# Performance work log

Hardware: AMD Instinct MI355X
Metric: run time of the kernel (lower is better)

## Reference

```python
import jax, jax.numpy as jnp
import numpy as np

B, T, C, H = 8, 2048, 1024, 1024
SCALE = 1.0 / np.sqrt(H).astype(np.float32)


def setup_inputs() -> dict:
    key = jax.random.key(0)
    kx, kq, kk, kv = jax.random.split(key, 4)
    x = jax.random.normal(kx, (B, T, C), dtype=jnp.float32)
    # Linear(C -> H, bias=False): store weights as [C, H] so y = x @ W
    Wq = jax.random.normal(kq, (C, H), dtype=jnp.float32) * (1.0 / np.sqrt(C))
    Wk = jax.random.normal(kk, (C, H), dtype=jnp.float32) * (1.0 / np.sqrt(C))
    Wv = jax.random.normal(kv, (C, H), dtype=jnp.float32) * (1.0 / np.sqrt(C))
    return {"x": x, "Wq": Wq, "Wk": Wk, "Wv": Wv}


def reference(x, Wq, Wk, Wv):
    # Projections
    Q = jnp.einsum('btc,ch->bth', x, Wq)
    K = jnp.einsum('btc,ch->bth', x, Wk)
    V = jnp.einsum('btc,ch->bth', x, Wv)
    t = x.shape[1]
    # Scaled dot-product scores with causal mask
    attn = jnp.einsum('bqh,bkh->bqk', Q, K) * SCALE  # [B,T,T]
    causal = jnp.tril(jnp.ones((t, t), dtype=bool))
    attn = jnp.where(causal, attn, -jnp.inf)
    scores = jax.nn.softmax(attn, axis=-1)
    # dropout p=0.0 (eval/deterministic) -> identity
    out = jnp.einsum('bqk,bkh->bqh', scores, V)
    return out
```

## Files before the change

kernel.cpp:

```cpp
#include <hip/hip_runtime.h>


typedef __attribute__((ext_vector_type(8))) __bf16 bf16x8;
typedef __attribute__((ext_vector_type(4))) float floatx4;

__device__ __forceinline__ unsigned short f2bf(float f) {
  unsigned int u = __float_as_uint(f);
  u += 0x7fffu + ((u >> 16) & 1u);
  return (unsigned short)(u >> 16);
}
__device__ __forceinline__ float bf2f(unsigned short s) {
  return __uint_as_float(((unsigned int)s) << 16);
}

__device__ __forceinline__ void gload_lds16(const unsigned short* g, unsigned short* l) {
  __builtin_amdgcn_global_load_lds(
      (const __attribute__((address_space(1))) void*)g,
      (__attribute__((address_space(3))) void*)l,
      16, 0, 0);
}

__device__ __forceinline__ void gemm_mainloop64(
    const unsigned short* __restrict__ A, int lda,
    const unsigned short* __restrict__ Bt, int ldb,
    int m0, int n0, int kSteps,
    unsigned short* As, unsigned short* Bs,
    floatx4 (&acc)[4][4])
{
  const int tid  = threadIdx.x;
  const int wave = tid >> 6;
  const int lane = tid & 63;
  const int wr = wave >> 1;
  const int wc = wave & 1;

  const int rowIn = lane >> 3;
  const int srcChunk = (((lane & 7) ^ rowIn) << 3);

  const unsigned short* gA = A  + (size_t)(m0 + wave * 32 + rowIn) * lda + srcChunk;
  const unsigned short* gB = Bt + (size_t)(n0 + wave * 32 + rowIn) * ldb + srcChunk;
  const int lda8 = lda << 3;
  const int ldb8 = ldb << 3;

  const int fr = lane & 15;
  const int kq = lane >> 4;
  const int ac0 = ((kq ^ (fr & 7)) << 3);
  const int ac1 = (((4 + kq) ^ (fr & 7)) << 3);

  for (int kt = 0; kt < kSteps; ++kt) {
    __syncthreads();
#pragma unroll
    for (int i = 0; i < 4; ++i)
      gload_lds16(gA + i * lda8, As + (wave * 32 + i * 8) * 64);
#pragma unroll
    for (int i = 0; i < 4; ++i)
      gload_lds16(gB + i * ldb8, Bs + (wave * 32 + i * 8) * 64);
    gA += 64; gB += 64;
    __syncthreads();

    bf16x8 af[4], bg[4];
#pragma unroll
    for (int i = 0; i < 4; ++i)
      af[i] = *(const bf16x8*)(As + (wr * 64 + i * 16 + fr) * 64 + ac0);
#pragma unroll
    for (int j = 0; j < 4; ++j)
      bg[j] = *(const bf16x8*)(Bs + (wc * 64 + j * 16 + fr) * 64 + ac0);
#pragma unroll
    for (int i = 0; i < 4; ++i)
#pragma unroll
      for (int j = 0; j < 4; ++j)
        acc[i][j] = __builtin_amdgcn_mfma_f32_16x16x32_bf16(af[i], bg[j], acc[i][j], 0, 0, 0);
#pragma unroll
    for (int i = 0; i < 4; ++i)
      af[i] = *(const bf16x8*)(As + (wr * 64 + i * 16 + fr) * 64 + ac1);
#pragma unroll
    for (int j = 0; j < 4; ++j)
      bg[j] = *(const bf16x8*)(Bs + (wc * 64 + j * 16 + fr) * 64 + ac1);
#pragma unroll
    for (int i = 0; i < 4; ++i)
#pragma unroll
      for (int j = 0; j < 4; ++j)
        acc[i][j] = __builtin_amdgcn_mfma_f32_16x16x32_bf16(af[i], bg[j], acc[i][j], 0, 0, 0);
  }
}

#define ACC_INIT(acc)                         \
  do {                                        \
    floatx4 z_ = {0.f, 0.f, 0.f, 0.f};        \
    _Pragma("unroll")                         \
    for (int i_ = 0; i_ < 4; ++i_)            \
      _Pragma("unroll")                       \
      for (int j_ = 0; j_ < 4; ++j_)          \
        acc[i_][j_] = z_;                     \
  } while (0)


__global__ __launch_bounds__(256) void prep_kernel(
    const float* __restrict__ x,
    const float* __restrict__ Wq,
    const float* __restrict__ Wk,
    const float* __restrict__ Wv,
    unsigned short* __restrict__ xb,
    unsigned short* __restrict__ Wt,
    float* __restrict__ l)
{
  const int bid = blockIdx.x;
  const int tid = threadIdx.x;
  if (bid < 16384) {
    int idx = (bid * 256 + tid) * 4;
    float4 v = *(const float4*)(x + idx);
    ushort4 o;
    o.x = f2bf(v.x); o.y = f2bf(v.y); o.z = f2bf(v.z); o.w = f2bf(v.w);
    *(ushort4*)(xb + idx) = o;
  } else if (bid < 17152) {
    __shared__ unsigned short tile[64][65];
    const int wb = bid - 16384;
    const float* W = (wb < 256) ? Wq : (wb < 512) ? Wk : Wv;
    unsigned short* Wtp = Wt + (size_t)(wb >> 8) * 1048576;
    const int rem = wb & 255;
    const int k0 = (rem & 15) * 64, n0 = (rem >> 4) * 64;
    const int tx = tid & 63, ty = tid >> 6;
#pragma unroll
    for (int r = 0; r < 64; r += 4)
      tile[r + ty][tx] = f2bf(W[(size_t)(k0 + r + ty) * 1024 + (n0 + tx)]);
    __syncthreads();
#pragma unroll
    for (int r = 0; r < 64; r += 4)
      Wtp[(size_t)(n0 + r + ty) * 1024 + (k0 + tx)] = tile[tx][r + ty];
  } else {
    l[(bid - 17152) * 256 + tid] = 0.f;
  }
}

__global__ __launch_bounds__(512, 2) void gemm_qkv_kernel(
    const unsigned short* __restrict__ xb,
    const unsigned short* __restrict__ Wt,
    unsigned short* __restrict__ Q,
    unsigned short* __restrict__ K,
    unsigned short* __restrict__ V)
{
  __shared__ __align__(16) unsigned short lds[49152];

  const int bid = blockIdx.x;
  const int xcd = bid & 7;
  const int local = bid >> 3;
  const int mi = xcd * 8 + (local & 7);
  const int ni = local >> 3;
  const int m0 = mi * 256;
  const int n0 = ni * 256;

  const int tid = threadIdx.x;
  const int w = tid >> 6;
  const int l = tid & 63;
  const int wr = w >> 2;
  const int wc = w & 3;

  const int sr0 = w * 16 + (l >> 2);
  const int scs = (((l & 3) ^ ((l >> 3) & 3)) << 3);

  const unsigned short* pA0 = xb + (size_t)(m0 + sr0) * 1024 + scs;
  const unsigned short* pA1 = xb + (size_t)(m0 + 128 + sr0) * 1024 + scs;
  const unsigned short* pB0 = Wt + (size_t)(n0 + sr0) * 1024 + scs;
  const unsigned short* pB1 = Wt + (size_t)(n0 + 128 + sr0) * 1024 + scs;

  const int stgW = w * 512;

#define STAGE4(slot)                                             \
  do {                                                           \
    unsigned short* _sA = &lds[(slot) * 8192 + stgW];            \
    unsigned short* _sB = &lds[24576 + (slot) * 8192 + stgW];    \
    gload_lds16(pA0, _sA);                                       \
    gload_lds16(pA1, _sA + 4096);                                \
    gload_lds16(pB0, _sB);                                       \
    gload_lds16(pB1, _sB + 4096);                                \
    pA0 += 32; pA1 += 32; pB0 += 32; pB1 += 32;                  \
  } while (0)

  const int fr = l & 15;
  const int q  = l >> 4;
  const int cks = ((q ^ ((fr >> 1) & 3)) << 3);
  const int aOff = (wr * 128 + fr) * 32 + cks;
  const int bOff = (wc * 64 + fr) * 32 + cks;

  floatx4 acc[8][4];
  {
    floatx4 z = {0.f, 0.f, 0.f, 0.f};
#pragma unroll
    for (int i = 0; i < 8; ++i)
#pragma unroll
      for (int j = 0; j < 4; ++j)
        acc[i][j] = z;
  }

  STAGE4(0);
  STAGE4(1);
  asm volatile("s_waitcnt vmcnt(4)" ::: "memory");
  __builtin_amdgcn_s_barrier();

  bf16x8 a[8], b0[4], b1[4];
  {
    const unsigned short* sA = &lds[0];
    const unsigned short* sB = &lds[24576];
#pragma unroll
    for (int j = 0; j < 4; ++j) b0[j] = *(const bf16x8*)(sB + bOff + j * 512);
    a[0] = *(const bf16x8*)(sA + aOff);
    a[1] = *(const bf16x8*)(sA + aOff + 512);
  }

#define MFMA_PAIR(I0, BU)                                                           \
  do {                                                                              \
    __builtin_amdgcn_s_setprio(1);                                                  \
    _Pragma("unroll")                                                               \
    for (int j = 0; j < 4; ++j) {                                                   \
      acc[(I0)][j] =                                                                \
          __builtin_amdgcn_mfma_f32_16x16x32_bf16(a[(I0)], BU[j], acc[(I0)][j], 0, 0, 0); \
      acc[(I0) + 1][j] =                                                            \
          __builtin_amdgcn_mfma_f32_16x16x32_bf16(a[(I0) + 1], BU[j], acc[(I0) + 1][j], 0, 0, 0); \
    }                                                                               \
    __builtin_amdgcn_s_setprio(0);                                                  \
  } while (0)

#define ITER(KT, BU, BP)                                                  \
  do {                                                                    \
    const int nslot = (slot == 2) ? 0 : slot + 1;                         \
    const int sslot = (nslot == 2) ? 0 : nslot + 1;                       \
    const unsigned short* sA  = &lds[slot * 8192];                        \
    const unsigned short* sAn = &lds[nslot * 8192];                       \
    const unsigned short* sBn = &lds[24576 + nslot * 8192];               \
    unsigned short* dA = &lds[sslot * 8192 + stgW];                       \
    unsigned short* dB = &lds[24576 + sslot * 8192 + stgW];               \
    const bool doStage = ((KT) < 30);                                     \
    const bool doNext  = ((KT) < 31);                                     \
    a[2] = *(const bf16x8*)(sA + aOff + 2 * 512);                         \
    a[3] = *(const bf16x8*)(sA + aOff + 3 * 512);                         \
    if (doStage) gload_lds16(pA0, dA);                                    \
    __builtin_amdgcn_s_barrier();                                         \
    MFMA_PAIR(0, BU);                                                     \
    __builtin_amdgcn_s_barrier();                                         \
    a[4] = *(const bf16x8*)(sA + aOff + 4 * 512);                         \
    a[5] = *(const bf16x8*)(sA + aOff + 5 * 512);                         \
    if (doStage) gload_lds16(pA1, dA + 4096);                             \
    __builtin_amdgcn_s_barrier();                                         \
    MFMA_PAIR(2, BU);                                                     \
    __builtin_amdgcn_s_barrier();                                         \
    a[6] = *(const bf16x8*)(sA + aOff + 6 * 512);                         \
    a[7] = *(const bf16x8*)(sA + aOff + 7 * 512);                         \
    if (doStage) gload_lds16(pB0, dB);                                    \
    __builtin_amdgcn_s_barrier();                                         \
    MFMA_PAIR(4, BU);                                                     \
    __builtin_amdgcn_s_barrier();                                         \
    if (doStage) STAGE_LAST(dB);                                          \
    if (doNext) {                                                         \
      if (doStage) asm volatile("s_waitcnt vmcnt(3)" ::: "memory");       \
      else         asm volatile("s_waitcnt vmcnt(0)" ::: "memory");       \
      __builtin_amdgcn_s_barrier();                                       \
      _Pragma("unroll")                                                   \
      for (int j = 0; j < 4; ++j)                                         \
        BP[j] = *(const bf16x8*)(sBn + bOff + j * 512);                   \
      a[0] = *(const bf16x8*)(sAn + aOff);                                \
      a[1] = *(const bf16x8*)(sAn + aOff + 512);                          \
    }                                                                     \
    MFMA_PAIR(6, BU);                                                     \
    __builtin_amdgcn_s_barrier();                                         \
    slot = nslot;                                                         \
  } while (0)

#define STAGE_LAST(dB)                                                    \
  do {                                                                    \
    gload_lds16(pB1, (dB) + 4096);                                        \
    pA0 += 32; pA1 += 32; pB0 += 32; pB1 += 32;                           \
  } while (0)

  int slot = 0;
#pragma unroll 1
  for (int kt2 = 0; kt2 < 16; ++kt2) {
    const int kt = kt2 * 2;
    ITER(kt, b0, b1);
    ITER(kt + 1, b1, b0);
  }
#undef ITER
#undef STAGE_LAST
#undef MFMA_PAIR
#undef STAGE4

  unsigned short* const dsts[3] = {Q, K, V};
  unsigned short* D = dsts[n0 >> 10];
  const int ncol0 = n0 & 1023;

  const int rb = m0 + wr * 128 + (q << 2);
  const int cb = ncol0 + wc * 64 + fr;
#pragma unroll
  for (int i = 0; i < 8; ++i)
#pragma unroll
    for (int j = 0; j < 4; ++j)
#pragma unroll
      for (int r = 0; r < 4; ++r)
        D[(size_t)(rb + i * 16 + r) * 1024 + (cb + j * 16)] = f2bf(acc[i][j][r]);
}

__global__ void transpose_v_kernel(const unsigned short* __restrict__ V,
                                   unsigned short* __restrict__ Vt) {
  __shared__ unsigned short tile[64][68];
  const int b = blockIdx.z;
  const int t0 = blockIdx.x * 64, h0 = blockIdx.y * 64;
  const int tid = threadIdx.x;
  const int cx = (tid & 15) * 4;
  const int ry = tid >> 4;
  const unsigned short* Vb = V + (size_t)b * 2048 * 1024;
#pragma unroll
  for (int r = 0; r < 64; r += 16) {
    ushort4 v = *(const ushort4*)(Vb + (size_t)(t0 + r + ry) * 1024 + (h0 + cx));
    *(ushort4*)&tile[r + ry][cx] = v;
  }
  __syncthreads();
  unsigned short* Vtb = Vt + (size_t)b * 1024 * 2048;
#pragma unroll
  for (int r = 0; r < 64; r += 16) {
    const int h = r + ry;
    ushort4 o;
    o.x = tile[cx][h]; o.y = tile[cx + 1][h]; o.z = tile[cx + 2][h]; o.w = tile[cx + 3][h];
    *(ushort4*)(Vtb + (size_t)(h0 + h) * 2048 + (t0 + cx)) = o;
  }
}

__global__ __launch_bounds__(256) void gemm_scores_kernel(
    const unsigned short* __restrict__ Q,
    const unsigned short* __restrict__ K,
    unsigned short* __restrict__ S,
    float* __restrict__ lsum)
{
  const int b = blockIdx.x & 7;
  const int t = blockIdx.x >> 3;
  int mi = (int)((sqrtf(8.f * (float)t + 1.f) - 1.f) * 0.5f);
  while ((mi + 1) * (mi + 2) / 2 <= t) ++mi;
  while (mi * (mi + 1) / 2 > t) --mi;
  const int ni = t - mi * (mi + 1) / 2;
  const int m0 = mi * 128;
  const int n0 = ni * 128;

  __shared__ __align__(16) unsigned short As[128 * 64];
  __shared__ __align__(16) unsigned short Bs[128 * 64];
  floatx4 acc[4][4];
  ACC_INIT(acc);
  const unsigned short* Qb = Q + (size_t)b * 2048 * 1024;
  const unsigned short* Kb = K + (size_t)b * 2048 * 1024;
  gemm_mainloop64(Qb, 1024, Kb, 1024, m0, n0, 16, As, Bs, acc);

  unsigned short* Sb = S + (size_t)b * 2048 * 2048;
  float* lb = lsum + b * 2048;
  const int tid = threadIdx.x, wave = tid >> 6, lane = tid & 63;
  const int wr = wave >> 1, wc = wave & 1;
  const int rb = m0 + wr * 64 + ((lane >> 4) << 2);
  const int cb = n0 + wc * 64 + (lane & 15);

  float rsum[4][4];
#pragma unroll
  for (int i = 0; i < 4; ++i)
#pragma unroll
    for (int r = 0; r < 4; ++r)
      rsum[i][r] = 0.f;

#pragma unroll
  for (int i = 0; i < 4; ++i)
#pragma unroll
    for (int j = 0; j < 4; ++j)
#pragma unroll
      for (int r = 0; r < 4; ++r) {
        const int tq = rb + i * 16 + r;
        const int tk = cb + j * 16;
        float e = 0.f;
        if (tk <= tq) e = __expf(acc[i][j][r] * 0.03125f);
        const unsigned short h = f2bf(e);
        Sb[(size_t)tq * 2048 + tk] = h;
        rsum[i][r] += bf2f(h);
      }

#pragma unroll
  for (int off = 1; off < 16; off <<= 1)
#pragma unroll
    for (int i = 0; i < 4; ++i)
#pragma unroll
      for (int r = 0; r < 4; ++r)
        rsum[i][r] += __shfl_xor(rsum[i][r], off, 64);

  if ((lane & 15) == 0) {
#pragma unroll
    for (int i = 0; i < 4; ++i)
#pragma unroll
      for (int r = 0; r < 4; ++r)
        atomicAdd(&lb[rb + i * 16 + r], rsum[i][r]);
  }
}

__global__ __launch_bounds__(256) void gemm_pv_kernel(
    const unsigned short* __restrict__ S,
    const unsigned short* __restrict__ Vt,
    const float* __restrict__ lsum,
    float* __restrict__ out)
{
  const int b = blockIdx.x & 7;
  const int r2 = blockIdx.x >> 3;
  const int mi = 15 - (r2 >> 3);
  const int ni = r2 & 7;
  const int m0 = mi * 128;
  const int n0 = ni * 128;

  __shared__ __align__(16) unsigned short As[128 * 64];
  __shared__ __align__(16) unsigned short Bs[128 * 64];
  floatx4 acc[4][4];
  ACC_INIT(acc);
  const unsigned short* Pb = S  + (size_t)b * 2048 * 2048;
  const unsigned short* Vb = Vt + (size_t)b * 1024 * 2048;
  const int kSteps = m0 / 64 + 2;
  gemm_mainloop64(Pb, 2048, Vb, 2048, m0, n0, kSteps, As, Bs, acc);

  float* Ob = out + (size_t)b * 2048 * 1024;
  const float* lb = lsum + b * 2048;
  const int tid = threadIdx.x, wave = tid >> 6, lane = tid & 63;
  const int wr = wave >> 1, wc = wave & 1;
  const int rb = m0 + wr * 64 + ((lane >> 4) << 2);
  const int cb = n0 + wc * 64 + (lane & 15);

  float inv[4][4];
#pragma unroll
  for (int i = 0; i < 4; ++i)
#pragma unroll
    for (int r = 0; r < 4; ++r)
      inv[i][r] = 1.0f / lb[rb + i * 16 + r];

#pragma unroll
  for (int i = 0; i < 4; ++i)
#pragma unroll
    for (int j = 0; j < 4; ++j)
#pragma unroll
      for (int r = 0; r < 4; ++r)
        Ob[(size_t)(rb + i * 16 + r) * 1024 + (cb + j * 16)] = acc[i][j][r] * inv[i][r];
}


extern "C" void kernel_launch(void* const* d_in, const int* in_sizes, int n_in,
                              void* d_out, int out_size, void* d_ws, size_t ws_size,
                              hipStream_t stream) {
  const float* x  = (const float*)d_in[0];
  const float* Wq = (const float*)d_in[1];
  const float* Wk = (const float*)d_in[2];
  const float* Wv = (const float*)d_in[3];
  float* out = (float*)d_out;

  char* ws = (char*)d_ws;
  unsigned short* xb  = (unsigned short*)(ws);
  unsigned short* Wt  = (unsigned short*)(ws + 33554432ull);
  unsigned short* Q   = (unsigned short*)(ws + 39845888ull);
  unsigned short* K   = (unsigned short*)(ws + 73400320ull);
  unsigned short* V   = (unsigned short*)(ws + 106954752ull);
  unsigned short* Vt  = (unsigned short*)(ws + 140509184ull);
  unsigned short* S   = (unsigned short*)(ws + 174063616ull);
  float*          l   = (float*)(ws + 241172480ull);

  prep_kernel<<<17216, 256, 0, stream>>>(x, Wq, Wk, Wv, xb, Wt, l);

  gemm_qkv_kernel<<<768, 512, 0, stream>>>(xb, Wt, Q, K, V);

  transpose_v_kernel<<<dim3(32, 16, 8), 256, 0, stream>>>(V, Vt);
  gemm_scores_kernel<<<8 * 136, 256, 0, stream>>>(Q, K, S, l);
  gemm_pv_kernel<<<1024, 256, 0, stream>>>(S, Vt, l, out);
}
```

Baseline: 350.7 us.

## Fuse V transpose into QKV epilogue and widen PV tiles to 128x256

The QKV GEMM epilogue now writes V directly in transposed layout (Vt), so the separate transpose kernel and its extra read and write of V are gone. The PV GEMM switches to 512-thread blocks with 128x256 output tiles through a new mainloop variant, which halves the block count and reuses each loaded P tile across twice as many columns. The transposed stores are 8-byte ushort4 writes strided by 2048 elements, so they coalesce worse than the old row-major stores. The larger PV tiles also reduce parallelism for the causal workload.

```diff
diff --git a/kernel.cpp b/kernel.cpp
--- a/kernel.cpp
+++ b/kernel.cpp
@@ -54,6 +54,69 @@
 #pragma unroll
     for (int i = 0; i < 4; ++i)
       gload_lds16(gB + i * ldb8, Bs + (wave * 32 + i * 8) * 64);
+    gA += 64; gB += 64;
+    __syncthreads();
+
+    bf16x8 af[4], bg[4];
+#pragma unroll
+    for (int i = 0; i < 4; ++i)
+      af[i] = *(const bf16x8*)(As + (wr * 64 + i * 16 + fr) * 64 + ac0);
+#pragma unroll
+    for (int j = 0; j < 4; ++j)
+      bg[j] = *(const bf16x8*)(Bs + (wc * 64 + j * 16 + fr) * 64 + ac0);
+#pragma unroll
+    for (int i = 0; i < 4; ++i)
+#pragma unroll
+      for (int j = 0; j < 4; ++j)
+        acc[i][j] = __builtin_amdgcn_mfma_f32_16x16x32_bf16(af[i], bg[j], acc[i][j], 0, 0, 0);
+#pragma unroll
+    for (int i = 0; i < 4; ++i)
+      af[i] = *(const bf16x8*)(As + (wr * 64 + i * 16 + fr) * 64 + ac1);
+#pragma unroll
+    for (int j = 0; j < 4; ++j)
+      bg[j] = *(const bf16x8*)(Bs + (wc * 64 + j * 16 + fr) * 64 + ac1);
+#pragma unroll
+    for (int i = 0; i < 4; ++i)
+#pragma unroll
+      for (int j = 0; j < 4; ++j)
+        acc[i][j] = __builtin_amdgcn_mfma_f32_16x16x32_bf16(af[i], bg[j], acc[i][j], 0, 0, 0);
+  }
+}
+
+__device__ __forceinline__ void gemm_mainloop64w(
+    const unsigned short* __restrict__ A, int lda,
+    const unsigned short* __restrict__ Bt, int ldb,
+    int m0, int n0, int kSteps,
+    unsigned short* As, unsigned short* Bs,
+    floatx4 (&acc)[4][4])
+{
+  const int tid  = threadIdx.x;
+  const int w    = tid >> 6;
+  const int lane = tid & 63;
+  const int wr = w >> 2;
+  const int wc = w & 3;
+
+  const int rowIn = lane >> 3;
+  const int srcChunk = (((lane & 7) ^ rowIn) << 3);
+
+  const unsigned short* gA = A  + (size_t)(m0 + w * 16 + rowIn) * lda + srcChunk;
+  const unsigned short* gB = Bt + (size_t)(n0 + w * 32 + rowIn) * ldb + srcChunk;
+  const int lda8 = lda << 3;
+  const int ldb8 = ldb << 3;
+
+  const int fr = lane & 15;
+  const int kq = lane >> 4;
+  const int ac0 = ((kq ^ (fr & 7)) << 3);
+  const int ac1 = (((4 + kq) ^ (fr & 7)) << 3);
+
+  for (int kt = 0; kt < kSteps; ++kt) {
+    __syncthreads();
+#pragma unroll
+    for (int i = 0; i < 2; ++i)
+      gload_lds16(gA + i * lda8, As + (w * 16 + i * 8) * 64);
+#pragma unroll
+    for (int i = 0; i < 4; ++i)
+      gload_lds16(gB + i * ldb8, Bs + (w * 32 + i * 8) * 64);
     gA += 64; gB += 64;
     __syncthreads();
 
@@ -136,7 +199,7 @@
     const unsigned short* __restrict__ Wt,
     unsigned short* __restrict__ Q,
     unsigned short* __restrict__ K,
-    unsigned short* __restrict__ V)
+    unsigned short* __restrict__ Vt)
 {
   __shared__ __align__(16) unsigned short lds[49152];
 
@@ -248,7 +311,10 @@
     __builtin_amdgcn_s_barrier();                                         \
     MFMA_PAIR(4, BU);                                                     \
     __builtin_amdgcn_s_barrier();                                         \
-    if (doStage) STAGE_LAST(dB);                                          \
+    if (doStage) {                                                        \
+      gload_lds16(pB1, dB + 4096);                                        \
+      pA0 += 32; pA1 += 32; pB0 += 32; pB1 += 32;                         \
+    }                                                                     \
     if (doNext) {                                                         \
       if (doStage) asm volatile("s_waitcnt vmcnt(3)" ::: "memory");       \
       else         asm volatile("s_waitcnt vmcnt(0)" ::: "memory");       \
@@ -264,12 +330,6 @@
     slot = nslot;                                                         \
   } while (0)
 
-#define STAGE_LAST(dB)                                                    \
-  do {                                                                    \
-    gload_lds16(pB1, (dB) + 4096);                                        \
-    pA0 += 32; pA1 += 32; pB0 += 32; pB1 += 32;                           \
-  } while (0)
-
   int slot = 0;
 #pragma unroll 1
   for (int kt2 = 0; kt2 < 16; ++kt2) {
@@ -278,47 +338,34 @@
     ITER(kt + 1, b1, b0);
   }
 #undef ITER
-#undef STAGE_LAST
 #undef MFMA_PAIR
 #undef STAGE4
 
-  unsigned short* const dsts[3] = {Q, K, V};
-  unsigned short* D = dsts[n0 >> 10];
-  const int ncol0 = n0 & 1023;
-
   const int rb = m0 + wr * 128 + (q << 2);
-  const int cb = ncol0 + wc * 64 + fr;
-#pragma unroll
-  for (int i = 0; i < 8; ++i)
-#pragma unroll
-    for (int j = 0; j < 4; ++j)
-#pragma unroll
-      for (int r = 0; r < 4; ++r)
-        D[(size_t)(rb + i * 16 + r) * 1024 + (cb + j * 16)] = f2bf(acc[i][j][r]);
-}
-
-__global__ void transpose_v_kernel(const unsigned short* __restrict__ V,
-                                   unsigned short* __restrict__ Vt) {
-  __shared__ unsigned short tile[64][68];
-  const int b = blockIdx.z;
-  const int t0 = blockIdx.x * 64, h0 = blockIdx.y * 64;
-  const int tid = threadIdx.x;
-  const int cx = (tid & 15) * 4;
-  const int ry = tid >> 4;
-  const unsigned short* Vb = V + (size_t)b * 2048 * 1024;
-#pragma unroll
-  for (int r = 0; r < 64; r += 16) {
-    ushort4 v = *(const ushort4*)(Vb + (size_t)(t0 + r + ry) * 1024 + (h0 + cx));
-    *(ushort4*)&tile[r + ry][cx] = v;
-  }
-  __syncthreads();
-  unsigned short* Vtb = Vt + (size_t)b * 1024 * 2048;
-#pragma unroll
-  for (int r = 0; r < 64; r += 16) {
-    const int h = r + ry;
-    ushort4 o;
-    o.x = tile[cx][h]; o.y = tile[cx + 1][h]; o.z = tile[cx + 2][h]; o.w = tile[cx + 3][h];
-    *(ushort4*)(Vtb + (size_t)(h0 + h) * 2048 + (t0 + cx)) = o;
+  const int cbl = wc * 64 + fr;
+  if (n0 < 2048) {
+    unsigned short* D = (n0 < 1024) ? Q : K;
+    const int cb = (n0 & 1023) + cbl;
+#pragma unroll
+    for (int i = 0; i < 8; ++i)
+#pragma unroll
+      for (int j = 0; j < 4; ++j)
+#pragma unroll
+        for (int r = 0; r < 4; ++r)
+          D[(size_t)(rb + i * 16 + r) * 1024 + (cb + j * 16)] = f2bf(acc[i][j][r]);
+  } else {
+    const size_t bb = (size_t)(rb >> 11) * (1024ull * 2048ull);
+    const int t0 = rb & 2047;
+    const int h0 = (n0 - 2048) + cbl;
+#pragma unroll
+    for (int i = 0; i < 8; ++i)
+#pragma unroll
+      for (int j = 0; j < 4; ++j) {
+        ushort4 o;
+        o.x = f2bf(acc[i][j][0]); o.y = f2bf(acc[i][j][1]);
+        o.z = f2bf(acc[i][j][2]); o.w = f2bf(acc[i][j][3]);
+        *(ushort4*)(Vt + bb + (size_t)(h0 + j * 16) * 2048 + (t0 + i * 16)) = o;
+      }
   }
 }
 
@@ -391,7 +438,7 @@
   }
 }
 
-__global__ __launch_bounds__(256) void gemm_pv_kernel(
+__global__ __launch_bounds__(512) void gemm_pv_kernel(
     const unsigned short* __restrict__ S,
     const unsigned short* __restrict__ Vt,
     const float* __restrict__ lsum,
@@ -399,24 +446,24 @@
 {
   const int b = blockIdx.x & 7;
   const int r2 = blockIdx.x >> 3;
-  const int mi = 15 - (r2 >> 3);
-  const int ni = r2 & 7;
+  const int mi = 15 - (r2 >> 2);
+  const int ni = r2 & 3;
   const int m0 = mi * 128;
-  const int n0 = ni * 128;
+  const int n0 = ni * 256;
 
   __shared__ __align__(16) unsigned short As[128 * 64];
-  __shared__ __align__(16) unsigned short Bs[128 * 64];
+  __shared__ __align__(16) unsigned short Bs[256 * 64];
   floatx4 acc[4][4];
   ACC_INIT(acc);
   const unsigned short* Pb = S  + (size_t)b * 2048 * 2048;
   const unsigned short* Vb = Vt + (size_t)b * 1024 * 2048;
   const int kSteps = m0 / 64 + 2;
-  gemm_mainloop64(Pb, 2048, Vb, 2048, m0, n0, kSteps, As, Bs, acc);
+  gemm_mainloop64w(Pb, 2048, Vb, 2048, m0, n0, kSteps, As, Bs, acc);
 
   float* Ob = out + (size_t)b * 2048 * 1024;
   const float* lb = lsum + b * 2048;
-  const int tid = threadIdx.x, wave = tid >> 6, lane = tid & 63;
-  const int wr = wave >> 1, wc = wave & 1;
+  const int tid = threadIdx.x, w = tid >> 6, lane = tid & 63;
+  const int wr = w >> 2, wc = w & 3;
   const int rb = m0 + wr * 64 + ((lane >> 4) << 2);
   const int cb = n0 + wc * 64 + (lane & 15);
 
@@ -451,16 +498,14 @@
   unsigned short* Wt  = (unsigned short*)(ws + 33554432ull);
   unsigned short* Q   = (unsigned short*)(ws + 39845888ull);
   unsigned short* K   = (unsigned short*)(ws + 73400320ull);
-  unsigned short* V   = (unsigned short*)(ws + 106954752ull);
-  unsigned short* Vt  = (unsigned short*)(ws + 140509184ull);
-  unsigned short* S   = (unsigned short*)(ws + 174063616ull);
-  float*          l   = (float*)(ws + 241172480ull);
+  unsigned short* Vt  = (unsigned short*)(ws + 106954752ull);
+  unsigned short* S   = (unsigned short*)(ws + 140509184ull);
+  float*          l   = (float*)(ws + 207618048ull);
 
   prep_kernel<<<17216, 256, 0, stream>>>(x, Wq, Wk, Wv, xb, Wt, l);
 
-  gemm_qkv_kernel<<<768, 512, 0, stream>>>(xb, Wt, Q, K, V);
-
-  transpose_v_kernel<<<dim3(32, 16, 8), 256, 0, stream>>>(V, Vt);
+  gemm_qkv_kernel<<<768, 512, 0, stream>>>(xb, Wt, Q, K, Vt);
+
   gemm_scores_kernel<<<8 * 136, 256, 0, stream>>>(Q, K, S, l);
-  gemm_pv_kernel<<<1024, 256, 0, stream>>>(S, Vt, l, out);
-}
+  gemm_pv_kernel<<<512, 512, 0, stream>>>(S, Vt, l, out);
+}
```

Result: no change. 352.9 us (+0.6%).

## Fuse V transpose into QKV epilogue and stage score tile through LDS

Applied to the files above, without the earlier changes.

The QKV GEMM epilogue now writes the V projection directly in transposed [B,H,T] layout using 4-wide vector stores, which removes the separate transpose kernel and its extra read and write of V. Separately, the scores kernel first writes its exp'd bf16 tile into swizzled shared memory and then stores it to global memory in 16-byte row chunks, replacing scattered 2-byte stores. This adds a barrier and LDS traffic to the scores epilogue. The transposed V writes from the QKV kernel are still only partly coalesced.

```diff
diff --git a/kernel.cpp b/kernel.cpp
--- a/kernel.cpp
+++ b/kernel.cpp
@@ -136,7 +136,7 @@
     const unsigned short* __restrict__ Wt,
     unsigned short* __restrict__ Q,
     unsigned short* __restrict__ K,
-    unsigned short* __restrict__ V)
+    unsigned short* __restrict__ Vt)
 {
   __shared__ __align__(16) unsigned short lds[49152];
 
@@ -248,7 +248,10 @@
     __builtin_amdgcn_s_barrier();                                         \
     MFMA_PAIR(4, BU);                                                     \
     __builtin_amdgcn_s_barrier();                                         \
-    if (doStage) STAGE_LAST(dB);                                          \
+    if (doStage) {                                                        \
+      gload_lds16(pB1, dB + 4096);                                        \
+      pA0 += 32; pA1 += 32; pB0 += 32; pB1 += 32;                         \
+    }                                                                     \
     if (doNext) {                                                         \
       if (doStage) asm volatile("s_waitcnt vmcnt(3)" ::: "memory");       \
       else         asm volatile("s_waitcnt vmcnt(0)" ::: "memory");       \
@@ -264,12 +267,6 @@
     slot = nslot;                                                         \
   } while (0)
 
-#define STAGE_LAST(dB)                                                    \
-  do {                                                                    \
-    gload_lds16(pB1, (dB) + 4096);                                        \
-    pA0 += 32; pA1 += 32; pB0 += 32; pB1 += 32;                           \
-  } while (0)
-
   int slot = 0;
 #pragma unroll 1
   for (int kt2 = 0; kt2 < 16; ++kt2) {
@@ -278,47 +275,34 @@
     ITER(kt + 1, b1, b0);
   }
 #undef ITER
-#undef STAGE_LAST
 #undef MFMA_PAIR
 #undef STAGE4
 
-  unsigned short* const dsts[3] = {Q, K, V};
-  unsigned short* D = dsts[n0 >> 10];
-  const int ncol0 = n0 & 1023;
-
   const int rb = m0 + wr * 128 + (q << 2);
-  const int cb = ncol0 + wc * 64 + fr;
-#pragma unroll
-  for (int i = 0; i < 8; ++i)
-#pragma unroll
-    for (int j = 0; j < 4; ++j)
-#pragma unroll
-      for (int r = 0; r < 4; ++r)
-        D[(size_t)(rb + i * 16 + r) * 1024 + (cb + j * 16)] = f2bf(acc[i][j][r]);
-}
-
-__global__ void transpose_v_kernel(const unsigned short* __restrict__ V,
-                                   unsigned short* __restrict__ Vt) {
-  __shared__ unsigned short tile[64][68];
-  const int b = blockIdx.z;
-  const int t0 = blockIdx.x * 64, h0 = blockIdx.y * 64;
-  const int tid = threadIdx.x;
-  const int cx = (tid & 15) * 4;
-  const int ry = tid >> 4;
-  const unsigned short* Vb = V + (size_t)b * 2048 * 1024;
-#pragma unroll
-  for (int r = 0; r < 64; r += 16) {
-    ushort4 v = *(const ushort4*)(Vb + (size_t)(t0 + r + ry) * 1024 + (h0 + cx));
-    *(ushort4*)&tile[r + ry][cx] = v;
-  }
-  __syncthreads();
-  unsigned short* Vtb = Vt + (size_t)b * 1024 * 2048;
-#pragma unroll
-  for (int r = 0; r < 64; r += 16) {
-    const int h = r + ry;
-    ushort4 o;
-    o.x = tile[cx][h]; o.y = tile[cx + 1][h]; o.z = tile[cx + 2][h]; o.w = tile[cx + 3][h];
-    *(ushort4*)(Vtb + (size_t)(h0 + h) * 2048 + (t0 + cx)) = o;
+  const int cbl = wc * 64 + fr;
+  if (n0 < 2048) {
+    unsigned short* D = (n0 < 1024) ? Q : K;
+    const int cb = (n0 & 1023) + cbl;
+#pragma unroll
+    for (int i = 0; i < 8; ++i)
+#pragma unroll
+      for (int j = 0; j < 4; ++j)
+#pragma unroll
+        for (int r = 0; r < 4; ++r)
+          D[(size_t)(rb + i * 16 + r) * 1024 + (cb + j * 16)] = f2bf(acc[i][j][r]);
+  } else {
+    const size_t bb = (size_t)(rb >> 11) * (1024ull * 2048ull);
+    const int t0 = rb & 2047;
+    const int h0 = (n0 - 2048) + cbl;
+#pragma unroll
+    for (int i = 0; i < 8; ++i)
+#pragma unroll
+      for (int j = 0; j < 4; ++j) {
+        ushort4 o;
+        o.x = f2bf(acc[i][j][0]); o.y = f2bf(acc[i][j][1]);
+        o.z = f2bf(acc[i][j][2]); o.w = f2bf(acc[i][j][3]);
+        *(ushort4*)(Vt + bb + (size_t)(h0 + j * 16) * 2048 + (t0 + i * 16)) = o;
+      }
   }
 }
 
@@ -337,20 +321,21 @@
   const int m0 = mi * 128;
   const int n0 = ni * 128;
 
-  __shared__ __align__(16) unsigned short As[128 * 64];
-  __shared__ __align__(16) unsigned short Bs[128 * 64];
+  __shared__ __align__(16) unsigned short lds[16384];
   floatx4 acc[4][4];
   ACC_INIT(acc);
   const unsigned short* Qb = Q + (size_t)b * 2048 * 1024;
   const unsigned short* Kb = K + (size_t)b * 2048 * 1024;
-  gemm_mainloop64(Qb, 1024, Kb, 1024, m0, n0, 16, As, Bs, acc);
+  gemm_mainloop64(Qb, 1024, Kb, 1024, m0, n0, 16, lds, lds + 8192, acc);
 
   unsigned short* Sb = S + (size_t)b * 2048 * 2048;
   float* lb = lsum + b * 2048;
   const int tid = threadIdx.x, wave = tid >> 6, lane = tid & 63;
   const int wr = wave >> 1, wc = wave & 1;
-  const int rb = m0 + wr * 64 + ((lane >> 4) << 2);
-  const int cb = n0 + wc * 64 + (lane & 15);
+  const int wrl = wr * 64 + ((lane >> 4) << 2);
+  const int wcl = wc * 64 + (lane & 15);
+
+  __syncthreads();
 
   float rsum[4][4];
 #pragma unroll
@@ -365,12 +350,12 @@
     for (int j = 0; j < 4; ++j)
 #pragma unroll
       for (int r = 0; r < 4; ++r) {
-        const int tq = rb + i * 16 + r;
-        const int tk = cb + j * 16;
+        const int row = wrl + i * 16 + r;
+        const int col = wcl + j * 16;
         float e = 0.f;
-        if (tk <= tq) e = __expf(acc[i][j][r] * 0.03125f);
+        if (n0 + col <= m0 + row) e = __expf(acc[i][j][r] * 0.03125f);
         const unsigned short h = f2bf(e);
-        Sb[(size_t)tq * 2048 + tk] = h;
+        lds[row * 128 + (col ^ ((row & 7) << 3))] = h;
         rsum[i][r] += bf2f(h);
       }
 
@@ -387,7 +372,24 @@
     for (int i = 0; i < 4; ++i)
 #pragma unroll
       for (int r = 0; r < 4; ++r)
-        atomicAdd(&lb[rb + i * 16 + r], rsum[i][r]);
+        atomicAdd(&lb[m0 + wrl + i * 16 + r], rsum[i][r]);
+  }
+
+  __syncthreads();
+
+  const int rgrp = tid >> 2;
+  const int cq = tid & 3;
+#pragma unroll
+  for (int rr = 0; rr < 2; ++rr) {
+    const int row = rr * 64 + rgrp;
+    const size_t rbase = (size_t)(m0 + row) * 2048 + n0;
+#pragma unroll
+    for (int k = 0; k < 4; ++k) {
+      const int chunk = cq + k * 4;
+      const int csw = chunk ^ (row & 7);
+      *(bf16x8*)(Sb + rbase + chunk * 8) =
+          *(const bf16x8*)(lds + row * 128 + csw * 8);
+    }
   }
 }
 
@@ -451,16 +453,14 @@
   unsigned short* Wt  = (unsigned short*)(ws + 33554432ull);
   unsigned short* Q   = (unsigned short*)(ws + 39845888ull);
   unsigned short* K   = (unsigned short*)(ws + 73400320ull);
-  unsigned short* V   = (unsigned short*)(ws + 106954752ull);
-  unsigned short* Vt  = (unsigned short*)(ws + 140509184ull);
-  unsigned short* S   = (unsigned short*)(ws + 174063616ull);
-  float*          l   = (float*)(ws + 241172480ull);
+  unsigned short* Vt  = (unsigned short*)(ws + 106954752ull);
+  unsigned short* S   = (unsigned short*)(ws + 140509184ull);
+  float*          l   = (float*)(ws + 207618048ull);
 
   prep_kernel<<<17216, 256, 0, stream>>>(x, Wq, Wk, Wv, xb, Wt, l);
 
-  gemm_qkv_kernel<<<768, 512, 0, stream>>>(xb, Wt, Q, K, V);
-
-  transpose_v_kernel<<<dim3(32, 16, 8), 256, 0, stream>>>(V, Vt);
+  gemm_qkv_kernel<<<768, 512, 0, stream>>>(xb, Wt, Q, K, Vt);
+
   gemm_scores_kernel<<<8 * 136, 256, 0, stream>>>(Q, K, S, l);
   gemm_pv_kernel<<<1024, 256, 0, stream>>>(S, Vt, l, out);
 }
```

After: 349.5 us. No clear change (-0.3%).
